# Kernel tuning notes

Measured on AMD Instinct MI355X. Metric: run time of the kernel, lower is better.

Reference implementation:

```python
import jax, jax.numpy as jnp
import numpy as np

EPS = 1e-7          # keras K.epsilon()
MIN_TEMP = 0.1
ALPHA = 0.99999
START_TEMP = 10.0
BATCH, D, BINS, K_OUT = 4096, 20000, 10, 64


def setup_inputs() -> dict:
    key = jax.random.key(0)
    k1, k2, k3 = jax.random.split(key, 3)
    X = jax.random.normal(k1, (BATCH, D), dtype=jnp.float32)
    u = jax.random.normal(k2, (D, BINS), dtype=jnp.float32)
    # keras 'uniform' initializer: U(-0.05, 0.05)
    tinyW = jax.random.uniform(k3, (BINS, K_OUT), dtype=jnp.float32, minval=-0.05, maxval=0.05)
    temp = jnp.float32(START_TEMP)
    return {"X": X, "u": u, "tinyW": tinyW, "temp": temp}


def greedy_assign(p):
    """Greedy bipartite argmax-and-mask assignment (the host loop in the original).
    p: (k, d) scores. Returns (k, d) 0/1 assignment with one 1 per row, unique cols."""
    k, d = p.shape

    def step(pm, _):
        ind = jnp.argmax(pm)            # global argmax over flattened (k, d)
        x = ind // d
        y = ind % d
        pm = pm.at[x, :].set(-1.0).at[:, y].set(-1.0)
        return pm, (x, y)

    _, (xs, ys) = jax.lax.scan(step, p, None, length=k)
    return jnp.zeros((k, d), p.dtype).at[xs, ys].set(1.0)


def reference(X, u, tinyW, temp):
    # al = softmax(u @ tinyW) over output_dim axis, then transpose -> (k, d)
    al = jax.nn.softmax(u @ tinyW, axis=-1).T                  # (k, d)
    logits = jnp.log(10.0 * jnp.clip(al, EPS, 0.9999999))      # (k, d)
    # Gumbel noise: -log(-log(U)), U ~ Uniform(eps, 1)
    nkey = jax.random.key(42)
    uniform = jax.random.uniform(nkey, logits.shape, logits.dtype, EPS, 1.0)
    gumbel = -jnp.log(-jnp.log(uniform))
    # annealed temperature update (K.update in original)
    new_temp = jnp.maximum(jnp.float32(MIN_TEMP), temp * jnp.float32(ALPHA))
    samples = jax.nn.softmax((logits + gumbel) / new_temp, axis=-1)  # (k, d)
    # inference-path discrete selection via greedy argmax-and-mask loop
    discrete = greedy_assign(samples)                           # (k, d)
    # training path: Y = X @ samples^T  (main memory-bound skinny GEMM)
    Y = X @ samples.T                                           # (batch, k)
    return Y, discrete, new_temp
```

## Files before the change

kernel.cpp:

```cpp
#include <hip/hip_runtime.h>
#include <stdint.h>
#include <math.h>

typedef unsigned long long ull;
typedef __attribute__((ext_vector_type(8))) short short8;
typedef __attribute__((ext_vector_type(4))) float f32x4;

#define DD 20000
#define NK 64
#define NB 4096
#define YN (NB * NK)
#define TOTN (YN + NK * DD + 1)
#define KS 32

#define E_OFF   0u
#define RSP_OFF 10240000u
#define CV_OFF  10400256u
#define CC_OFF  10416640u
#define SB_OFF  10433024u
#define P_OFF   12993024u

__device__ __forceinline__ uint32_t tf_bits(uint32_t j) {
  const uint32_t k0 = 0u, k1 = 42u;
  const uint32_t k2 = 0x1BD11BDAu ^ k0 ^ k1;
  uint32_t x0 = k0;
  uint32_t x1 = j + k1;
#define TFR(r) { x0 += x1; x1 = (x1 << r) | (x1 >> (32 - r)); x1 ^= x0; }
  TFR(13) TFR(15) TFR(26) TFR(6)
  x0 += k1; x1 += k2 + 1u;
  TFR(17) TFR(29) TFR(16) TFR(24)
  x0 += k2; x1 += k0 + 2u;
  TFR(13) TFR(15) TFR(26) TFR(6)
  x0 += k0; x1 += k1 + 3u;
  TFR(17) TFR(29) TFR(16) TFR(24)
  x0 += k1; x1 += k2 + 4u;
  TFR(13) TFR(15) TFR(26) TFR(6)
  x0 += k2; x1 += k0 + 5u;
#undef TFR
  return x0 ^ x1;
}

__global__ __launch_bounds__(256) void k_z(
    const float* __restrict__ uu, const float* __restrict__ tw,
    const float* __restrict__ temp, double* __restrict__ E,
    double* __restrict__ RSP) {
  __shared__ double tile[NK][65];
  __shared__ double psumw[4][NK];
  const int tid = threadIdx.x;
  const int lane = tid & 63;
  const int wv = tid >> 6;
  const int d0 = blockIdx.x * 64;
  const float nt = fmaxf(0.1f, temp[0] * 0.99999f);
  float w[10];
#pragma unroll
  for (int i = 0; i < 10; ++i) w[i] = tw[i * NK + lane];
  double psum = 0.0;
  for (int it = 0; it < 16; ++it) {
    const int dl = wv * 16 + it;
    const int d = d0 + dl;
    double e = 0.0;
    if (d < DD) {
      float m = 0.f;
#pragma unroll
      for (int i = 0; i < 10; ++i) m = fmaf(uu[d * 10 + i], w[i], m);
      float mx = m;
#pragma unroll
      for (int off = 32; off; off >>= 1) mx = fmaxf(mx, __shfl_xor(mx, off, 64));
      double ee = exp((double)(m - mx));
      double ssum = ee;
#pragma unroll
      for (int off = 32; off; off >>= 1) ssum += __shfl_xor(ssum, off, 64);
      float al = (float)(ee / ssum);
      float c = fminf(fmaxf(al, 1e-7f), 0.9999999f);
      float lg = (float)log((double)(10.0f * c));
      const uint32_t bits = tf_bits((uint32_t)(lane * DD + d));
      float uf = __uint_as_float((bits >> 9) | 0x3f800000u) - 1.0f;
      float uv = fmaxf(1e-7f, uf * (1.0f - 1e-7f) + 1e-7f);
      float g = (float)(-log(-log((double)uv)));
      float z = (lg + g) / nt;
      e = exp((double)z);
    }
    tile[lane][dl] = e;
    psum += e;
  }
  psumw[wv][lane] = psum;
  __syncthreads();
  for (int r0 = 0; r0 < NK; r0 += 4) {
    const int r = r0 + wv;
    const int d = d0 + lane;
    if (d < DD) E[(size_t)r * DD + d] = tile[r][lane];
  }
  if (wv == 0) {
    double s = psumw[0][lane] + psumw[1][lane] + psumw[2][lane] + psumw[3][lane];
    RSP[(size_t)blockIdx.x * NK + lane] = s;
  }
}

__global__ __launch_bounds__(256) void k_rows(
    const double* __restrict__ E, const double* __restrict__ RSP,
    ushort* __restrict__ SBm, float* __restrict__ disc,
    float* __restrict__ cv, int* __restrict__ cc) {
  const int k = blockIdx.x;
  const int tid = threadIdx.x;
  __shared__ double redd[256];
  __shared__ ull keys[2048];
  __shared__ ull wbest[4];
  const double* er = E + (size_t)k * DD;
  ushort* sbr = SBm + (size_t)k * DD;
  float* dr = disc + (size_t)k * DD;
  double psum = 0.0;
  for (int b = tid; b < 313; b += 256) psum += RSP[(size_t)b * NK + k];
  redd[tid] = psum;
  __syncthreads();
  for (int s = 128; s; s >>= 1) {
    if (tid < s) redd[tid] += redd[tid + s];
    __syncthreads();
  }
  const double sumall = redd[0];
  float tv[8]; int tc[8];
#pragma unroll
  for (int s = 0; s < 8; ++s) { tv[s] = -1.f; tc[s] = 0; }
  for (int d = tid; d < DD; d += 256) {
    float svv = (float)(er[d] / sumall);
    uint32_t ub = __float_as_uint(svv);
    sbr[d] = (ushort)((ub + 0x7FFFu + ((ub >> 16) & 1u)) >> 16);
    dr[d] = 0.f;
    if (svv > tv[7]) {
      float cvr = svv; int ccr = d;
#pragma unroll
      for (int s = 0; s < 8; ++s) {
        bool sw = cvr > tv[s];
        float nv = sw ? cvr : tv[s]; int nc = sw ? ccr : tc[s];
        cvr = sw ? tv[s] : cvr; ccr = sw ? tc[s] : ccr;
        tv[s] = nv; tc[s] = nc;
      }
    }
  }
#pragma unroll
  for (int s = 0; s < 8; ++s)
    keys[(tid << 3) + s] = (((ull)__float_as_uint(tv[s])) << 32)
                         | ((ull)(uint32_t)(32767 - tc[s]) << 11)
                         | ((ull)tid << 3) | (ull)s;
  __syncthreads();
  for (int t = 0; t < NK; ++t) {
    ull best = 0;
#pragma unroll
    for (int s = 0; s < 8; ++s) { ull kk = keys[(tid << 3) + s]; if (kk > best) best = kk; }
#pragma unroll
    for (int off = 32; off; off >>= 1) { ull o = __shfl_xor(best, off, 64); if (o > best) best = o; }
    if ((tid & 63) == 0) wbest[tid >> 6] = best;
    __syncthreads();
    ull win = wbest[0];
#pragma unroll
    for (int wI = 1; wI < 4; ++wI) if (wbest[wI] > win) win = wbest[wI];
    const uint32_t lo = (uint32_t)win;
    const int slot = lo & 7;
    const int owner = (lo >> 3) & 255;
    const int col = 32767 - (int)(lo >> 11);
    if (tid == 0) {
      cv[(k << 6) + t] = __uint_as_float((uint32_t)(win >> 32));
      cc[(k << 6) + t] = col;
    }
    if (tid == owner) keys[(owner << 3) + slot] = 0;
    __syncthreads();
  }
}

__global__ __launch_bounds__(64) void k_greedy(
    const float* __restrict__ cv, const int* __restrict__ cc,
    const float* __restrict__ temp, float* __restrict__ out) {
  __shared__ float v[NK][NK];
  __shared__ int c[NK][NK];
  __shared__ unsigned char used[DD];
  const int lane = threadIdx.x;
  for (int i = lane; i < DD; i += 64) used[i] = 0;
  for (int i = 0; i < NK; ++i) { v[i][lane] = cv[(i << 6) + lane]; c[i][lane] = cc[(i << 6) + lane]; }
  __syncthreads();
  int ptr = 0;
  bool done = false;
  for (int t = 0; t < NK; ++t) {
    ull key = 0;
    if (!done) {
      while (ptr < NK && used[c[lane][ptr]]) ++ptr;
      if (ptr < NK) {
        key = (((ull)__float_as_uint(v[lane][ptr])) << 21)
            | ((ull)(uint32_t)(63 - lane) << 15)
            | (ull)(uint32_t)(32767 - c[lane][ptr]);
      }
    }
#pragma unroll
    for (int off = 32; off; off >>= 1) { ull o = __shfl_xor(key, off, 64); if (o > key) key = o; }
    const int col = 32767 - (int)(key & 0x7FFF);
    const int row = 63 - (int)((key >> 15) & 63);
    if (lane == row) done = true;
    if (lane == 0) { used[col] = 1; out[YN + (size_t)row * DD + col] = 1.0f; }
    __syncthreads();
  }
  if (lane == 0) out[TOTN - 1] = fmaxf(0.1f, temp[0] * 0.99999f);
}

__global__ __launch_bounds__(256) void k_gemm(
    const float* __restrict__ X, const ushort* __restrict__ SBm,
    float* __restrict__ P) {
  const int tid = threadIdx.x;
  const int lane = tid & 63;
  const int wv = tid >> 6;
  const int ksp = blockIdx.x;
  const int m16 = lane & 15;
  const int kq = lane >> 4;
  const int mRow = blockIdx.y * 64 + wv * 16 + m16;
  const float* xp = X + (size_t)mRow * DD;
  const ushort* bp = SBm + (size_t)m16 * DD;
  f32x4 acc[4] = {{0,0,0,0},{0,0,0,0},{0,0,0,0},{0,0,0,0}};
#pragma unroll 2
  for (int s = ksp; s < 625; s += KS) {
    const int k0 = s * 32 + kq * 8;
    const float4 xa = *(const float4*)(xp + k0);
    const float4 xb = *(const float4*)(xp + k0 + 4);
    union { uint32_t u[4]; short8 v; } A;
    uint32_t ua0 = __float_as_uint(xa.x), ua1 = __float_as_uint(xa.y);
    uint32_t ua2 = __float_as_uint(xa.z), ua3 = __float_as_uint(xa.w);
    uint32_t ub0 = __float_as_uint(xb.x), ub1 = __float_as_uint(xb.y);
    uint32_t ub2 = __float_as_uint(xb.z), ub3 = __float_as_uint(xb.w);
    ua0 = (ua0 + 0x7FFFu + ((ua0 >> 16) & 1u)) >> 16;
    ua1 = (ua1 + 0x7FFFu + ((ua1 >> 16) & 1u)) >> 16;
    ua2 = (ua2 + 0x7FFFu + ((ua2 >> 16) & 1u)) >> 16;
    ua3 = (ua3 + 0x7FFFu + ((ua3 >> 16) & 1u)) >> 16;
    ub0 = (ub0 + 0x7FFFu + ((ub0 >> 16) & 1u)) >> 16;
    ub1 = (ub1 + 0x7FFFu + ((ub1 >> 16) & 1u)) >> 16;
    ub2 = (ub2 + 0x7FFFu + ((ub2 >> 16) & 1u)) >> 16;
    ub3 = (ub3 + 0x7FFFu + ((ub3 >> 16) & 1u)) >> 16;
    A.u[0] = ua0 | (ua1 << 16); A.u[1] = ua2 | (ua3 << 16);
    A.u[2] = ub0 | (ub1 << 16); A.u[3] = ub2 | (ub3 << 16);
#pragma unroll
    for (int nt = 0; nt < 4; ++nt) {
      union { uint4 q; short8 v; } B;
      B.q = *(const uint4*)(bp + (size_t)nt * 16 * DD + k0);
      acc[nt] = __builtin_amdgcn_mfma_f32_16x16x32_bf16(A.v, B.v, acc[nt], 0, 0, 0);
    }
  }
  float* pp = P + (size_t)ksp * YN;
  const int rBase = blockIdx.y * 64 + wv * 16 + kq * 4;
#pragma unroll
  for (int nt = 0; nt < 4; ++nt)
#pragma unroll
    for (int r = 0; r < 4; ++r)
      pp[(size_t)(rBase + r) * 64 + nt * 16 + m16] = acc[nt][r];
}

__global__ __launch_bounds__(256) void k_gred(const float* __restrict__ P,
                                              float* __restrict__ Y) {
  const int i = blockIdx.x * 256 + threadIdx.x;
  float4 a = ((const float4*)P)[i];
#pragma unroll
  for (int j = 1; j < KS; ++j) {
    const float4 b = ((const float4*)(P + (size_t)j * YN))[i];
    a.x += b.x; a.y += b.y; a.z += b.z; a.w += b.w;
  }
  ((float4*)Y)[i] = a;
}

extern "C" void kernel_launch(void* const* d_in, const int* in_sizes, int n_in,
                              void* d_out, int out_size, void* d_ws, size_t ws_size,
                              hipStream_t stream) {
  (void)in_sizes; (void)n_in; (void)out_size; (void)ws_size;
  const float* X = (const float*)d_in[0];
  const float* uu = (const float*)d_in[1];
  const float* tw = (const float*)d_in[2];
  const float* temp = (const float*)d_in[3];
  float* out = (float*)d_out;
  char* W = (char*)d_ws;
  double* E   = (double*)(W + E_OFF);
  double* RSP = (double*)(W + RSP_OFF);
  float*  CV  = (float*)(W + CV_OFF);
  int*    CC  = (int*)(W + CC_OFF);
  ushort* SBm = (ushort*)(W + SB_OFF);
  float*  P   = (float*)(W + P_OFF);

  hipLaunchKernelGGL(k_z, dim3(313), dim3(256), 0, stream, uu, tw, temp, E, RSP);
  hipLaunchKernelGGL(k_rows, dim3(64), dim3(256), 0, stream, E, RSP, SBm, out + YN, CV, CC);
  hipLaunchKernelGGL(k_greedy, dim3(1), dim3(64), 0, stream, CV, CC, temp, out);
  hipLaunchKernelGGL(k_gemm, dim3(KS, 64), dim3(256), 0, stream, X, SBm, P);
  hipLaunchKernelGGL(k_gred, dim3(256), dim3(256), 0, stream, P, out);
}
```

Measured before the change: 650.8 us.

## Feed GEMM unnormalized exp values and apply row normalization in the reduce kernel

The bf16 B matrix for the GEMM is now built from the unnormalized exponentials in k_z, so the GEMM no longer waits for k_rows. The per-row 1/sum is applied in the final split-K reduction instead. Zeroing of the discrete output moves into k_z as float4 stores. The split-K factor is halved, which halves partial-sum traffic but gives fewer blocks. B loads are hoisted ahead of the A conversion, and greedy shared-memory loads are vectorised. Quantizing unnormalized values to bf16 before scaling can change rounding slightly.

Result: no change. 649.2 us (-0.2%).

```diff
diff --git a/kernel.cpp b/kernel.cpp
--- a/kernel.cpp
+++ b/kernel.cpp
@@ -11,14 +11,15 @@
 #define NB 4096
 #define YN (NB * NK)
 #define TOTN (YN + NK * DD + 1)
-#define KS 32
+#define KS 16
 
 #define E_OFF   0u
 #define RSP_OFF 10240000u
 #define CV_OFF  10400256u
 #define CC_OFF  10416640u
-#define SB_OFF  10433024u
-#define P_OFF   12993024u
+#define EB_OFF  10433024u
+#define IRS_OFF 12993024u
+#define P_OFF   12993280u
 
 __device__ __forceinline__ uint32_t tf_bits(uint32_t j) {
   const uint32_t k0 = 0u, k1 = 42u;
@@ -43,7 +44,8 @@
 __global__ __launch_bounds__(256) void k_z(
     const float* __restrict__ uu, const float* __restrict__ tw,
     const float* __restrict__ temp, double* __restrict__ E,
-    double* __restrict__ RSP) {
+    ushort* __restrict__ EB, double* __restrict__ RSP,
+    float* __restrict__ disc) {
   __shared__ double tile[NK][65];
   __shared__ double psumw[4][NK];
   const int tid = threadIdx.x;
@@ -88,26 +90,35 @@
   for (int r0 = 0; r0 < NK; r0 += 4) {
     const int r = r0 + wv;
     const int d = d0 + lane;
-    if (d < DD) E[(size_t)r * DD + d] = tile[r][lane];
+    if (d < DD) {
+      const double ev = tile[r][lane];
+      E[(size_t)r * DD + d] = ev;
+      const float ef = (float)ev;
+      uint32_t ub = __float_as_uint(ef);
+      EB[(size_t)r * DD + d] = (ushort)((ub + 0x7FFFu + ((ub >> 16) & 1u)) >> 16);
+    }
   }
   if (wv == 0) {
     double s = psumw[0][lane] + psumw[1][lane] + psumw[2][lane] + psumw[3][lane];
     RSP[(size_t)blockIdx.x * NK + lane] = s;
   }
+  const int cg = tid & 15;
+  const int r0 = tid >> 4;
+  if (d0 + cg * 4 < DD) {
+    for (int r = r0; r < NK; r += 16)
+      *(float4*)(disc + (size_t)r * DD + d0 + cg * 4) = make_float4(0.f, 0.f, 0.f, 0.f);
+  }
 }
 
 __global__ __launch_bounds__(256) void k_rows(
     const double* __restrict__ E, const double* __restrict__ RSP,
-    ushort* __restrict__ SBm, float* __restrict__ disc,
-    float* __restrict__ cv, int* __restrict__ cc) {
+    float* __restrict__ cv, int* __restrict__ cc, float* __restrict__ invRS) {
   const int k = blockIdx.x;
   const int tid = threadIdx.x;
   __shared__ double redd[256];
   __shared__ ull keys[2048];
   __shared__ ull wbest[4];
   const double* er = E + (size_t)k * DD;
-  ushort* sbr = SBm + (size_t)k * DD;
-  float* dr = disc + (size_t)k * DD;
   double psum = 0.0;
   for (int b = tid; b < 313; b += 256) psum += RSP[(size_t)b * NK + k];
   redd[tid] = psum;
@@ -117,14 +128,12 @@
     __syncthreads();
   }
   const double sumall = redd[0];
+  if (tid == 0) invRS[k] = (float)(1.0 / sumall);
   float tv[8]; int tc[8];
 #pragma unroll
   for (int s = 0; s < 8; ++s) { tv[s] = -1.f; tc[s] = 0; }
   for (int d = tid; d < DD; d += 256) {
     float svv = (float)(er[d] / sumall);
-    uint32_t ub = __float_as_uint(svv);
-    sbr[d] = (ushort)((ub + 0x7FFFu + ((ub >> 16) & 1u)) >> 16);
-    dr[d] = 0.f;
     if (svv > tv[7]) {
       float cvr = svv; int ccr = d;
 #pragma unroll
@@ -169,23 +178,26 @@
 __global__ __launch_bounds__(64) void k_greedy(
     const float* __restrict__ cv, const int* __restrict__ cc,
     const float* __restrict__ temp, float* __restrict__ out) {
-  __shared__ float v[NK][NK];
-  __shared__ int c[NK][NK];
+  __shared__ float vf[NK * NK];
+  __shared__ int cf[NK * NK];
   __shared__ unsigned char used[DD];
   const int lane = threadIdx.x;
   for (int i = lane; i < DD; i += 64) used[i] = 0;
-  for (int i = 0; i < NK; ++i) { v[i][lane] = cv[(i << 6) + lane]; c[i][lane] = cc[(i << 6) + lane]; }
+  for (int i = lane; i < 1024; i += 64) {
+    ((float4*)vf)[i] = ((const float4*)cv)[i];
+    ((int4*)cf)[i] = ((const int4*)cc)[i];
+  }
   __syncthreads();
   int ptr = 0;
   bool done = false;
   for (int t = 0; t < NK; ++t) {
     ull key = 0;
     if (!done) {
-      while (ptr < NK && used[c[lane][ptr]]) ++ptr;
+      while (ptr < NK && used[cf[(lane << 6) + ptr]]) ++ptr;
       if (ptr < NK) {
-        key = (((ull)__float_as_uint(v[lane][ptr])) << 21)
+        key = (((ull)__float_as_uint(vf[(lane << 6) + ptr])) << 21)
             | ((ull)(uint32_t)(63 - lane) << 15)
-            | (ull)(uint32_t)(32767 - c[lane][ptr]);
+            | (ull)(uint32_t)(32767 - cf[(lane << 6) + ptr]);
       }
     }
 #pragma unroll
@@ -200,7 +212,7 @@
 }
 
 __global__ __launch_bounds__(256) void k_gemm(
-    const float* __restrict__ X, const ushort* __restrict__ SBm,
+    const float* __restrict__ X, const ushort* __restrict__ EB,
     float* __restrict__ P) {
   const int tid = threadIdx.x;
   const int lane = tid & 63;
@@ -210,13 +222,17 @@
   const int kq = lane >> 4;
   const int mRow = blockIdx.y * 64 + wv * 16 + m16;
   const float* xp = X + (size_t)mRow * DD;
-  const ushort* bp = SBm + (size_t)m16 * DD;
+  const ushort* bp = EB + (size_t)m16 * DD;
   f32x4 acc[4] = {{0,0,0,0},{0,0,0,0},{0,0,0,0},{0,0,0,0}};
 #pragma unroll 2
   for (int s = ksp; s < 625; s += KS) {
     const int k0 = s * 32 + kq * 8;
     const float4 xa = *(const float4*)(xp + k0);
     const float4 xb = *(const float4*)(xp + k0 + 4);
+    union { uint4 q[4]; short8 v[4]; } B;
+#pragma unroll
+    for (int nt = 0; nt < 4; ++nt)
+      B.q[nt] = *(const uint4*)(bp + (size_t)nt * 16 * DD + k0);
     union { uint32_t u[4]; short8 v; } A;
     uint32_t ua0 = __float_as_uint(xa.x), ua1 = __float_as_uint(xa.y);
     uint32_t ua2 = __float_as_uint(xa.z), ua3 = __float_as_uint(xa.w);
@@ -233,11 +249,8 @@
     A.u[0] = ua0 | (ua1 << 16); A.u[1] = ua2 | (ua3 << 16);
     A.u[2] = ub0 | (ub1 << 16); A.u[3] = ub2 | (ub3 << 16);
 #pragma unroll
-    for (int nt = 0; nt < 4; ++nt) {
-      union { uint4 q; short8 v; } B;
-      B.q = *(const uint4*)(bp + (size_t)nt * 16 * DD + k0);
-      acc[nt] = __builtin_amdgcn_mfma_f32_16x16x32_bf16(A.v, B.v, acc[nt], 0, 0, 0);
-    }
+    for (int nt = 0; nt < 4; ++nt)
+      acc[nt] = __builtin_amdgcn_mfma_f32_16x16x32_bf16(A.v, B.v[nt], acc[nt], 0, 0, 0);
   }
   float* pp = P + (size_t)ksp * YN;
   const int rBase = blockIdx.y * 64 + wv * 16 + kq * 4;
@@ -249,6 +262,7 @@
 }
 
 __global__ __launch_bounds__(256) void k_gred(const float* __restrict__ P,
+                                              const float* __restrict__ invRS,
                                               float* __restrict__ Y) {
   const int i = blockIdx.x * 256 + threadIdx.x;
   float4 a = ((const float4*)P)[i];
@@ -257,6 +271,8 @@
     const float4 b = ((const float4*)(P + (size_t)j * YN))[i];
     a.x += b.x; a.y += b.y; a.z += b.z; a.w += b.w;
   }
+  const float4 irs = *(const float4*)(invRS + ((i * 4) & 63));
+  a.x *= irs.x; a.y *= irs.y; a.z *= irs.z; a.w *= irs.w;
   ((float4*)Y)[i] = a;
 }
 
@@ -274,12 +290,13 @@
   double* RSP = (double*)(W + RSP_OFF);
   float*  CV  = (float*)(W + CV_OFF);
   int*    CC  = (int*)(W + CC_OFF);
-  ushort* SBm = (ushort*)(W + SB_OFF);
+  ushort* EB  = (ushort*)(W + EB_OFF);
+  float*  IRS = (float*)(W + IRS_OFF);
   float*  P   = (float*)(W + P_OFF);
 
-  hipLaunchKernelGGL(k_z, dim3(313), dim3(256), 0, stream, uu, tw, temp, E, RSP);
-  hipLaunchKernelGGL(k_rows, dim3(64), dim3(256), 0, stream, E, RSP, SBm, out + YN, CV, CC);
+  hipLaunchKernelGGL(k_z, dim3(313), dim3(256), 0, stream, uu, tw, temp, E, EB, RSP, out + YN);
+  hipLaunchKernelGGL(k_gemm, dim3(KS, 64), dim3(256), 0, stream, X, EB, P);
+  hipLaunchKernelGGL(k_rows, dim3(64), dim3(256), 0, stream, E, RSP, CV, CC, IRS);
   hipLaunchKernelGGL(k_greedy, dim3(1), dim3(64), 0, stream, CV, CC, temp, out);
-  hipLaunchKernelGGL(k_gemm, dim3(KS, 64), dim3(256), 0, stream, X, SBm, P);
-  hipLaunchKernelGGL(k_gred, dim3(256), dim3(256), 0, stream, P, out);
-}
+  hipLaunchKernelGGL(k_gred, dim3(256), dim3(256), 0, stream, P, IRS, out);
+}
```
